# Kernel tuning notes

Hardware: AMD Instinct MI355X
Metric: run time of the kernel (lower is better)

Reference implementation:

```python
import jax, jax.numpy as jnp
import numpy as np

EMBED_DIM = 2048
NUM_HEADS = 16
HEAD_DIM = EMBED_DIM // NUM_HEADS
WINDOW = 512  # window_size; also used as chunk size (S must be a multiple)


def setup_inputs() -> dict:
    key = jax.random.key(0)
    k1, k2, k3 = jax.random.split(key, 3)
    B, S = 2, 4096
    x = jax.random.normal(k1, (B, S, EMBED_DIM), dtype=jnp.float32)
    w_qkv = jax.random.normal(k2, (3 * EMBED_DIM, EMBED_DIM), dtype=jnp.float32) * 0.02
    w_out = jax.random.normal(k3, (EMBED_DIM, EMBED_DIM), dtype=jnp.float32) * 0.02
    return {"x": x, "w_qkv": w_qkv, "w_out": w_out}


def _sliding_window_attn(q, k, v, window):
    # q,k,v: [B,H,S,d]; causal sliding window: kv valid iff 0 <= q_idx - kv_idx <= window.
    # Chunked O(S*window): each query chunk of size C=window attends to its own
    # chunk and the previous one (exactly covers the band of width window+1).
    B, H, S, d = q.shape
    C = window
    nc = S // C
    qc = q.reshape(B, H, nc, C, d)

    def two_chunks(t):
        tc = t.reshape(B, H, nc, C, d)
        prev = jnp.pad(tc[:, :, :-1], ((0, 0), (0, 0), (1, 0), (0, 0), (0, 0)))
        return jnp.concatenate([prev, tc], axis=3)  # [B,H,nc,2C,d]

    kc = two_chunks(k)
    vc = two_chunks(v)

    scale = 1.0 / np.sqrt(d).astype(np.float32)
    scores = jnp.einsum('bhnid,bhnjd->bhnij', qc, kc) * scale  # [B,H,nc,C,2C]

    i = jnp.arange(C)[:, None]            # local query index
    j = jnp.arange(2 * C)[None, :]        # local kv index within the 2-chunk span
    band = (j >= i) & (j <= i + C)        # causal & within window (C == window)
    kv_global = (jnp.arange(nc)[:, None, None] - 1) * C + j[None]  # [nc,1,2C]
    mask = band[None] & (kv_global >= 0)  # [nc,C,2C]; drops padded chunk 0 keys

    scores = jnp.where(mask[None, None], scores, jnp.finfo(scores.dtype).min)
    probs = jax.nn.softmax(scores, axis=-1)
    out = jnp.einsum('bhnij,bhnjd->bhnid', probs, vc)  # [B,H,nc,C,d]
    return out.reshape(B, H, S, d)


def reference(x, w_qkv, w_out):
    B, S, E = x.shape
    qkv = jnp.einsum('bse,fe->bsf', x, w_qkv)                       # [B,S,3E]
    qkv = qkv.reshape(B, S, 3, NUM_HEADS, HEAD_DIM)
    qkv = jnp.transpose(qkv, (2, 0, 3, 1, 4))                        # [3,B,H,S,d]
    q, k, v = qkv[0], qkv[1], qkv[2]
    attn = _sliding_window_attn(q, k, v, WINDOW)                     # [B,H,S,d]
    attn = jnp.transpose(attn, (0, 2, 1, 3)).reshape(B, S, E)
    return jnp.einsum('bse,fe->bsf', attn, w_out)
```

## Files before the change

### kernel.cpp

```cpp
#include <hip/hip_runtime.h>
#include <hip/hip_bf16.h>
#include <math.h>


#define SEQ   4096
#define BATCH 2
#define EMBED 2048
#define HEADS 16
#define HDIM  128
#define NELEM (BATCH * SEQ * EMBED)
#define SCL2E (0.088388347648318447f * 1.4426950408889634f)

typedef __attribute__((ext_vector_type(8))) short short8;
typedef __attribute__((ext_vector_type(4))) float f32x4;

__device__ __forceinline__ unsigned short f2bf(float f) {
    unsigned int u = __float_as_uint(f);
    u = (u + 0x7fff + ((u >> 16) & 1)) >> 16;
    return (unsigned short)u;
}

__device__ __forceinline__ unsigned int cvt_pk_bf16(float a, float b) {
    unsigned int r;
    asm volatile("v_cvt_pk_bf16_f32 %0, %1, %2" : "=v"(r) : "v"(a), "v"(b));
    return r;
}

__global__ void cast_bf16_kernel(const float* __restrict__ src,
                                 unsigned short* __restrict__ dst, int n8)
{
    const int i = blockIdx.x * blockDim.x + threadIdx.x;
    if (i >= n8) return;
    const float4 v0 = ((const float4*)src)[2 * i];
    const float4 v1 = ((const float4*)src)[2 * i + 1];
    union { unsigned short us[8]; uint4 u4; } o;
    o.us[0] = f2bf(v0.x); o.us[1] = f2bf(v0.y); o.us[2] = f2bf(v0.z); o.us[3] = f2bf(v0.w);
    o.us[4] = f2bf(v1.x); o.us[5] = f2bf(v1.y); o.us[6] = f2bf(v1.z); o.us[7] = f2bf(v1.w);
    ((uint4*)dst)[i] = o.u4;
}

template <int MODE>
__global__ __launch_bounds__(512, 2)
void gemm256_kernel(const unsigned short* __restrict__ A,
                    const unsigned short* __restrict__ B,
                    float* __restrict__ C,
                    unsigned short* __restrict__ P0,
                    unsigned short* __restrict__ P1,
                    int M, int N, int K)
{
    __shared__ __align__(16) char lds[131072];

    const int tid  = threadIdx.x;
    const int lane = tid & 63;
    const int w    = tid >> 6;
    const int wm   = w >> 2;
    const int wn   = w & 3;
    const int l16  = lane & 15;
    const int kg   = lane >> 4;

    const int nwg  = gridDim.x * gridDim.y;
    const int bidl = blockIdx.y * gridDim.x + blockIdx.x;
    const int cpx  = nwg >> 3;
    const int swzb = (bidl & 7) * cpx + (bidl >> 3);
    const int m0   = (swzb / gridDim.x) * 256;
    const int n0   = (swzb % gridDim.x) * 256;

    const int srow = w * 8 + (lane >> 3);
    const int sch8 = ((lane & 7) ^ (lane >> 3)) * 8;

    auto stage = [&](const unsigned short* X, int rowbase, int t2, int ldsbase) {
#pragma unroll
        for (int u = 0; u < 2; ++u) {
            const unsigned short* g = X + (size_t)(rowbase + u * 64 + srow) * K
                                      + t2 * 64 + sch8;
            unsigned int lb = __builtin_amdgcn_readfirstlane(
                (unsigned int)(uintptr_t)(lds + ldsbase + u * 8192 + w * 1024));
            asm volatile("s_mov_b32 m0, %0\n\t"
                         "global_load_lds_dwordx4 %1, off"
                         :: "s"(lb), "v"(g) : "memory");
        }
    };
    auto rdA = [&](int p, int mf, int ks) -> short8 {
        return *(const short8*)(lds + p * 65536 + (wm * 128 + mf * 16 + l16) * 128
                                + (((ks * 4 + kg) ^ (l16 & 7)) << 4));
    };
    auto rdB = [&](int p, int nf, int ks) -> short8 {
        return *(const short8*)(lds + 32768 + p * 65536
                                + (wn * 64 + nf * 16 + l16) * 128
                                + (((ks * 4 + kg) ^ (l16 & 7)) << 4));
    };

    f32x4 acc[8][4];
#pragma unroll
    for (int i = 0; i < 8; ++i)
#pragma unroll
        for (int j = 0; j < 4; ++j) acc[i][j] = (f32x4)0.f;

    const int NT = K >> 6;

    stage(B, n0 + 0,   0, 32768);
    stage(B, n0 + 128, 0, 32768 + 16384);
    stage(A, m0 + 0,   0, 0);
    stage(A, m0 + 128, 0, 16384);
    stage(B, n0 + 0,   1, 32768 + 65536);
    stage(B, n0 + 128, 1, 32768 + 65536 + 16384);
    asm volatile("s_waitcnt vmcnt(4)" ::: "memory");
    asm volatile("s_barrier" ::: "memory");

    short8 bfr[4][2];
    for (int t = 0; t < NT; ++t) {
        const int p = t & 1;
#pragma unroll
        for (int q = 0; q < 4; ++q) {
            short8 afr[2][2];
#pragma unroll
            for (int i = 0; i < 2; ++i)
#pragma unroll
                for (int ks = 0; ks < 2; ++ks)
                    afr[i][ks] = rdA(p, 2 * q + i, ks);
            if (q == 0) {
#pragma unroll
                for (int nf = 0; nf < 4; ++nf)
#pragma unroll
                    for (int ks = 0; ks < 2; ++ks)
                        bfr[nf][ks] = rdB(p, nf, ks);
            }
            if (q == 0)      { if (t + 1 < NT) stage(A, m0 + 0,   t + 1, (p ^ 1) * 65536); }
            else if (q == 1) { if (t + 1 < NT) stage(A, m0 + 128, t + 1, (p ^ 1) * 65536 + 16384); }
            else if (q == 2) { if (t + 2 < NT) stage(B, n0 + 0,   t + 2, p * 65536 + 32768); }
            else             { if (t + 2 < NT) stage(B, n0 + 128, t + 2, p * 65536 + 32768 + 16384); }

            asm volatile("s_barrier" ::: "memory");
            __builtin_amdgcn_s_setprio(1);
#pragma unroll
            for (int i = 0; i < 2; ++i)
#pragma unroll
                for (int nf = 0; nf < 4; ++nf)
#pragma unroll
                    for (int ks = 0; ks < 2; ++ks)
                        acc[2 * q + i][nf] = __builtin_amdgcn_mfma_f32_16x16x32_bf16(
                            afr[i][ks], bfr[nf][ks], acc[2 * q + i][nf], 0, 0, 0);
            __builtin_amdgcn_s_setprio(0);
            if (q == 3) {
                if (t >= NT - 2) asm volatile("s_waitcnt vmcnt(0)" ::: "memory");
                else             asm volatile("s_waitcnt vmcnt(4)" ::: "memory");
            }
            asm volatile("s_barrier" ::: "memory");
        }
    }

    if (MODE == 1) {
        const int cb = n0 + wn * 64;
        unsigned short* dst = (cb >> 11) ? P1 : P0;
        const int h  = (cb >> 7) & 15;
        const int db = cb & 127;
#pragma unroll
        for (int fi = 0; fi < 8; ++fi)
#pragma unroll
            for (int r = 0; r < 4; ++r) {
                const int mrow = m0 + wm * 128 + fi * 16 + kg * 4 + r;
                const int b = mrow >> 12, s = mrow & 4095;
                unsigned short* drow = dst + ((size_t)((b << 4) + h) * SEQ + s) * HDIM
                                       + db + l16;
#pragma unroll
                for (int nf = 0; nf < 4; ++nf) drow[nf * 16] = f2bf(acc[fi][nf][r]);
            }
    } else if (MODE == 2) {
#pragma unroll
        for (int fi = 0; fi < 8; ++fi)
#pragma unroll
            for (int r = 0; r < 4; ++r) {
                const int mrow = m0 + wm * 128 + fi * 16 + kg * 4 + r;
                const int h = mrow >> 7, d = mrow & 127;
#pragma unroll
                for (int nf = 0; nf < 4; ++nf) {
                    const int col = n0 + wn * 64 + nf * 16 + l16;
                    const int b = col >> 12, s = col & 4095;
                    const int sl = s & 63;
                    const int c = (sl & 0x23) | ((sl & 0x0C) << 1) | ((sl & 0x10) >> 2);
                    P0[((size_t)((b << 4) + h) * HDIM + d) * SEQ + (s & ~63) + c] =
                        f2bf(acc[fi][nf][r]);
                }
            }
    } else {
#pragma unroll
        for (int fi = 0; fi < 8; ++fi)
#pragma unroll
            for (int r = 0; r < 4; ++r) {
                float* crow = C + (size_t)(m0 + wm * 128 + fi * 16 + kg * 4 + r) * N
                              + n0 + wn * 64 + l16;
#pragma unroll
                for (int nf = 0; nf < 4; ++nf) crow[nf * 16] = acc[fi][nf][r];
            }
    }
}

__global__ __launch_bounds__(512)
void swa_mfma_kernel(const unsigned short* __restrict__ Qg,
                     const unsigned short* __restrict__ Kg,
                     const unsigned short* __restrict__ Vtg,
                     unsigned short* __restrict__ O )
{
    __shared__ __align__(16) char lds[32768];

    const int bid = blockIdx.x;
    const int qt  = bid & 31;
    const int h   = (bid >> 5) & 15;
    const int b   = bid >> 9;
    const int q0  = qt * 128;
    const int tid  = threadIdx.x;
    const int w    = tid >> 6;
    const int lane = tid & 63;
    const int l16  = lane & 15;
    const int kg   = lane >> 4;
    const size_t base = (size_t)((b << 4) + h) * SEQ * HDIM;
    const int gq = q0 + w * 16 + l16;

    short8 qf[4];
#pragma unroll
    for (int kw = 0; kw < 4; ++kw)
        qf[kw] = *(const short8*)(Qg + base + (size_t)gq * HDIM + kw * 32 + kg * 8);

    f32x4 acc_o[8];
#pragma unroll
    for (int db = 0; db < 8; ++db) acc_o[db] = (f32x4)0.f;
    float m = -1e30f, l = 0.f;

    for (int kt = 0; kt < 10; ++kt) {
        const int gk0 = q0 - 512 + kt * 64;
        if (gk0 < 0) continue;

#pragma unroll
        for (int u = 0; u < 2; ++u) {
            {
                const int id  = u * 512 + w * 64 + lane;
                const int row = id >> 4, ch = id & 15;
                const char* g = (const char*)(Kg + base + (size_t)(gk0 + row) * HDIM
                                              + ((ch ^ (row & 7)) << 3));
                unsigned int lb = __builtin_amdgcn_readfirstlane(
                    (unsigned int)(uintptr_t)(lds + u * 8192 + w * 1024));
                asm volatile("s_mov_b32 m0, %0\n\t"
                             "global_load_lds_dwordx4 %1, off"
                             :: "s"(lb), "v"(g) : "memory");
            }
            {
                const int id  = u * 512 + w * 64 + lane;
                const int d   = id >> 3, ch = id & 7;
                const char* g = (const char*)(Vtg + base + (size_t)d * SEQ + gk0
                                              + ((ch ^ (d & 7)) << 3));
                unsigned int lb = __builtin_amdgcn_readfirstlane(
                    (unsigned int)(uintptr_t)(lds + 16384 + u * 8192 + w * 1024));
                asm volatile("s_mov_b32 m0, %0\n\t"
                             "global_load_lds_dwordx4 %1, off"
                             :: "s"(lb), "v"(g) : "memory");
            }
        }
        asm volatile("s_waitcnt vmcnt(0)" ::: "memory");
        __syncthreads();

        const int qlo = q0 + w * 16;
        const bool active = (gk0 <= qlo + 15) && (gk0 + 63 >= qlo - 512);
        if (active) {
            f32x4 s4[4];
#pragma unroll
            for (int kb = 0; kb < 4; ++kb) s4[kb] = (f32x4)0.f;
#pragma unroll
            for (int kw = 0; kw < 4; ++kw)
#pragma unroll
                for (int kb = 0; kb < 4; ++kb) {
                    short8 kf = *(const short8*)(lds + (kb * 16 + l16) * 256
                                                 + (((kw * 4 + kg) ^ (l16 & 7)) << 4));
                    s4[kb] = __builtin_amdgcn_mfma_f32_16x16x32_bf16(
                        kf, qf[kw], s4[kb], 0, 0, 0);
                }

            const int dq = gq - gk0;
            float p[4][4];
            float tm = -1e30f;
#pragma unroll
            for (int kb = 0; kb < 4; ++kb)
#pragma unroll
                for (int r = 0; r < 4; ++r) {
                    const int koff = kb * 16 + kg * 4 + r;
                    const bool valid = (koff <= dq) && (koff >= dq - 512);
                    const float sv = valid ? s4[kb][r] * SCL2E : -1e30f;
                    p[kb][r] = sv;
                    tm = fmaxf(tm, sv);
                }
            tm = fmaxf(tm, __shfl_xor(tm, 16));
            tm = fmaxf(tm, __shfl_xor(tm, 32));
            const float mn   = fmaxf(m, tm);
            const float corr = __builtin_amdgcn_exp2f(m - mn);
            m = mn;
            l *= corr;
            float cr[4];
#pragma unroll
            for (int r = 0; r < 4; ++r) cr[r] = __shfl(corr, kg * 4 + r);
#pragma unroll
            for (int db = 0; db < 8; ++db)
#pragma unroll
                for (int r = 0; r < 4; ++r) acc_o[db][r] *= cr[r];

            float ts = 0.f;
#pragma unroll
            for (int kb = 0; kb < 4; ++kb)
#pragma unroll
                for (int r = 0; r < 4; ++r) {
                    const float pv = (p[kb][r] > -1e29f)
                                         ? __builtin_amdgcn_exp2f(p[kb][r] - m) : 0.f;
                    p[kb][r] = pv;
                    ts += pv;
                }
            ts += __shfl_xor(ts, 16);
            ts += __shfl_xor(ts, 32);
            l += ts;

            unsigned int dw[4][2];
#pragma unroll
            for (int kb = 0; kb < 4; ++kb) {
                dw[kb][0] = cvt_pk_bf16(p[kb][0], p[kb][1]);
                dw[kb][1] = cvt_pk_bf16(p[kb][2], p[kb][3]);
            }
#pragma unroll
            for (int w2 = 0; w2 < 2; ++w2) {
                union { unsigned int u[4]; short8 v; } pu;
                pu.u[0] = dw[2 * w2][0];     pu.u[1] = dw[2 * w2][1];
                pu.u[2] = dw[2 * w2 + 1][0]; pu.u[3] = dw[2 * w2 + 1][1];
#pragma unroll
                for (int db = 0; db < 8; ++db) {
                    short8 vf = *(const short8*)(lds + 16384 + (db * 16 + l16) * 128
                                                 + (((w2 * 4 + kg) ^ (l16 & 7)) << 4));
                    acc_o[db] = __builtin_amdgcn_mfma_f32_16x16x32_bf16(
                        pu.v, vf, acc_o[db], 0, 0, 0);
                }
            }
        }
        __syncthreads();
    }

    const float inv = 1.0f / l;
    float li[4];
#pragma unroll
    for (int r = 0; r < 4; ++r) li[r] = __shfl(inv, kg * 4 + r);
#pragma unroll
    for (int db = 0; db < 8; ++db)
#pragma unroll
        for (int r = 0; r < 4; ++r) {
            const int gqr = q0 + w * 16 + kg * 4 + r;
            O[((size_t)b * SEQ + gqr) * EMBED + h * HDIM + db * 16 + l16] =
                f2bf(acc_o[db][r] * li[r]);
        }
}

extern "C" void kernel_launch(void* const* d_in, const int* in_sizes, int n_in,
                              void* d_out, int out_size, void* d_ws, size_t ws_size,
                              hipStream_t stream)
{
    const float* x     = (const float*)d_in[0];
    const float* w_qkv = (const float*)d_in[1];
    const float* w_out = (const float*)d_in[2];
    float* out = (float*)d_out;

    char* ws = (char*)d_ws;
    unsigned short* xb    = (unsigned short*)(ws);
    unsigned short* wqkvb = (unsigned short*)(ws + 33554432);
    unsigned short* woutb = (unsigned short*)(ws + 58720256);
    unsigned short* qb    = (unsigned short*)(ws + 67108864);
    unsigned short* kb    = (unsigned short*)(ws + 100663296);
    unsigned short* vtb   = (unsigned short*)(ws + 134217728);
    unsigned short* attnb = (unsigned short*)(ws + 167772160);

    const int M = BATCH * SEQ;
    dim3 blk(256);

    hipLaunchKernelGGL(cast_bf16_kernel, dim3(NELEM / 8 / 256), blk, 0, stream,
                       x, xb, NELEM / 8);
    hipLaunchKernelGGL(cast_bf16_kernel, dim3(3 * EMBED * EMBED / 8 / 256), blk, 0, stream,
                       w_qkv, wqkvb, 3 * EMBED * EMBED / 8);
    hipLaunchKernelGGL(cast_bf16_kernel, dim3(EMBED * EMBED / 8 / 256), blk, 0, stream,
                       w_out, woutb, EMBED * EMBED / 8);

    hipLaunchKernelGGL((gemm256_kernel<1>), dim3(16, 32), dim3(512), 0, stream,
                       xb, wqkvb, (float*)nullptr, qb, kb, M, 2 * EMBED, EMBED);

    hipLaunchKernelGGL((gemm256_kernel<2>), dim3(32, 8), dim3(512), 0, stream,
                       wqkvb + (size_t)2 * EMBED * EMBED, xb, (float*)nullptr,
                       vtb, (unsigned short*)nullptr, EMBED, M, EMBED);

    hipLaunchKernelGGL(swa_mfma_kernel, dim3(BATCH * HEADS * (SEQ / 128)), dim3(512),
                       0, stream, qb, kb, vtb, attnb);

    hipLaunchKernelGGL((gemm256_kernel<0>), dim3(8, 32), dim3(512), 0, stream,
                       attnb, woutb, out, (unsigned short*)nullptr,
                       (unsigned short*)nullptr, M, EMBED, EMBED);
}
```

Before: 404.1 us.

## Software-pipeline GEMM fragment loads and double-buffer KV tiles in attention

The GEMM kernel's LDS layout changes to separate A and B double buffers (32KB each), so A fragments for the next quarter and next k-tile load from LDS while the current MFMAs run. It also swaps the block swizzle so consecutive blocks walk down M within an N column. The attention kernel double-buffers its K/V tiles in 64KB of LDS, prefetching the next tile before computing the current one. It also skips fully masked leading tiles by starting at a computed kt and drops the trailing syncthreads. The aim is to hide LDS and global load latency behind MFMA work, at the cost of more registers and LDS, which may lower occupancy.

```diff
diff --git a/kernel.cpp b/kernel.cpp
--- a/kernel.cpp
+++ b/kernel.cpp
@@ -62,8 +62,9 @@
     const int bidl = blockIdx.y * gridDim.x + blockIdx.x;
     const int cpx  = nwg >> 3;
     const int swzb = (bidl & 7) * cpx + (bidl >> 3);
-    const int m0   = (swzb / gridDim.x) * 256;
-    const int n0   = (swzb % gridDim.x) * 256;
+    const int MB   = gridDim.y;
+    const int n0   = (swzb / MB) * 256;
+    const int m0   = (swzb % MB) * 256;
 
     const int srow = w * 8 + (lane >> 3);
     const int sch8 = ((lane & 7) ^ (lane >> 3)) * 8;
@@ -81,11 +82,11 @@
         }
     };
     auto rdA = [&](int p, int mf, int ks) -> short8 {
-        return *(const short8*)(lds + p * 65536 + (wm * 128 + mf * 16 + l16) * 128
+        return *(const short8*)(lds + p * 32768 + (wm * 128 + mf * 16 + l16) * 128
                                 + (((ks * 4 + kg) ^ (l16 & 7)) << 4));
     };
     auto rdB = [&](int p, int nf, int ks) -> short8 {
-        return *(const short8*)(lds + 32768 + p * 65536
+        return *(const short8*)(lds + 65536 + p * 32768
                                 + (wn * 64 + nf * 16 + l16) * 128
                                 + (((ks * 4 + kg) ^ (l16 & 7)) << 4));
     };
@@ -98,56 +99,86 @@
 
     const int NT = K >> 6;
 
-    stage(B, n0 + 0,   0, 32768);
-    stage(B, n0 + 128, 0, 32768 + 16384);
     stage(A, m0 + 0,   0, 0);
     stage(A, m0 + 128, 0, 16384);
-    stage(B, n0 + 0,   1, 32768 + 65536);
-    stage(B, n0 + 128, 1, 32768 + 65536 + 16384);
-    asm volatile("s_waitcnt vmcnt(4)" ::: "memory");
+    stage(B, n0 + 0,   0, 65536);
+    stage(B, n0 + 128, 0, 65536 + 16384);
+    if (NT > 1) {
+        stage(B, n0 + 0,   1, 65536 + 32768);
+        stage(B, n0 + 128, 1, 65536 + 32768 + 16384);
+        asm volatile("s_waitcnt vmcnt(4)" ::: "memory");
+    } else {
+        asm volatile("s_waitcnt vmcnt(0)" ::: "memory");
+    }
     asm volatile("s_barrier" ::: "memory");
 
-    short8 bfr[4][2];
+    short8 afrA[2][2], afrB[2][2], bfr[4][2];
+#pragma unroll
+    for (int i = 0; i < 2; ++i)
+#pragma unroll
+        for (int ks = 0; ks < 2; ++ks) afrA[i][ks] = rdA(0, i, ks);
+#pragma unroll
+    for (int nf = 0; nf < 4; ++nf)
+#pragma unroll
+        for (int ks = 0; ks < 2; ++ks) bfr[nf][ks] = rdB(0, nf, ks);
+
+#define MFMA_QUAD(Q, FR)                                                        \
+    __builtin_amdgcn_s_setprio(1);                                              \
+    _Pragma("unroll")                                                           \
+    for (int i = 0; i < 2; ++i)                                                 \
+        _Pragma("unroll")                                                       \
+        for (int nf = 0; nf < 4; ++nf)                                          \
+            _Pragma("unroll")                                                   \
+            for (int ks = 0; ks < 2; ++ks)                                      \
+                acc[2 * (Q) + i][nf] = __builtin_amdgcn_mfma_f32_16x16x32_bf16( \
+                    FR[i][ks], bfr[nf][ks], acc[2 * (Q) + i][nf], 0, 0, 0);     \
+    __builtin_amdgcn_s_setprio(0);
+
     for (int t = 0; t < NT; ++t) {
         const int p = t & 1;
-#pragma unroll
-        for (int q = 0; q < 4; ++q) {
-            short8 afr[2][2];
+        if (t + 1 < NT) stage(A, m0 + 0, t + 1, (p ^ 1) * 32768);
+        asm volatile("s_barrier" ::: "memory");
+#pragma unroll
+        for (int i = 0; i < 2; ++i)
+#pragma unroll
+            for (int ks = 0; ks < 2; ++ks) afrB[i][ks] = rdA(p, 2 + i, ks);
+        MFMA_QUAD(0, afrA)
+        if (t + 1 < NT) stage(A, m0 + 128, t + 1, (p ^ 1) * 32768 + 16384);
+        asm volatile("s_barrier" ::: "memory");
+#pragma unroll
+        for (int i = 0; i < 2; ++i)
+#pragma unroll
+            for (int ks = 0; ks < 2; ++ks) afrA[i][ks] = rdA(p, 4 + i, ks);
+        MFMA_QUAD(1, afrB)
+        if (t + 2 < NT) stage(B, n0 + 0, t + 2, 65536 + p * 32768);
+        asm volatile("s_barrier" ::: "memory");
+#pragma unroll
+        for (int i = 0; i < 2; ++i)
+#pragma unroll
+            for (int ks = 0; ks < 2; ++ks) afrB[i][ks] = rdA(p, 6 + i, ks);
+        MFMA_QUAD(2, afrA)
+        if (t + 2 < NT) {
+            stage(B, n0 + 128, t + 2, 65536 + p * 32768 + 16384);
+            asm volatile("s_waitcnt vmcnt(4)" ::: "memory");
+        } else {
+            asm volatile("s_waitcnt vmcnt(0)" ::: "memory");
+        }
+        asm volatile("s_barrier" ::: "memory");
+        if (t + 1 < NT) {
 #pragma unroll
             for (int i = 0; i < 2; ++i)
 #pragma unroll
-                for (int ks = 0; ks < 2; ++ks)
-                    afr[i][ks] = rdA(p, 2 * q + i, ks);
-            if (q == 0) {
-#pragma unroll
-                for (int nf = 0; nf < 4; ++nf)
-#pragma unroll
-                    for (int ks = 0; ks < 2; ++ks)
-                        bfr[nf][ks] = rdB(p, nf, ks);
-            }
-            if (q == 0)      { if (t + 1 < NT) stage(A, m0 + 0,   t + 1, (p ^ 1) * 65536); }
-            else if (q == 1) { if (t + 1 < NT) stage(A, m0 + 128, t + 1, (p ^ 1) * 65536 + 16384); }
-            else if (q == 2) { if (t + 2 < NT) stage(B, n0 + 0,   t + 2, p * 65536 + 32768); }
-            else             { if (t + 2 < NT) stage(B, n0 + 128, t + 2, p * 65536 + 32768 + 16384); }
-
-            asm volatile("s_barrier" ::: "memory");
-            __builtin_amdgcn_s_setprio(1);
-#pragma unroll
-            for (int i = 0; i < 2; ++i)
-#pragma unroll
-                for (int nf = 0; nf < 4; ++nf)
-#pragma unroll
-                    for (int ks = 0; ks < 2; ++ks)
-                        acc[2 * q + i][nf] = __builtin_amdgcn_mfma_f32_16x16x32_bf16(
-                            afr[i][ks], bfr[nf][ks], acc[2 * q + i][nf], 0, 0, 0);
-            __builtin_amdgcn_s_setprio(0);
-            if (q == 3) {
-                if (t >= NT - 2) asm volatile("s_waitcnt vmcnt(0)" ::: "memory");
-                else             asm volatile("s_waitcnt vmcnt(4)" ::: "memory");
-            }
-            asm volatile("s_barrier" ::: "memory");
+                for (int ks = 0; ks < 2; ++ks) afrA[i][ks] = rdA(p ^ 1, i, ks);
+        }
+        MFMA_QUAD(3, afrB)
+        if (t + 1 < NT) {
+#pragma unroll
+            for (int nf = 0; nf < 4; ++nf)
+#pragma unroll
+                for (int ks = 0; ks < 2; ++ks) bfr[nf][ks] = rdB(p ^ 1, nf, ks);
         }
     }
+#undef MFMA_QUAD
 
     if (MODE == 1) {
         const int cb = n0 + wn * 64;
@@ -201,7 +232,7 @@
                      const unsigned short* __restrict__ Vtg,
                      unsigned short* __restrict__ O )
 {
-    __shared__ __align__(16) char lds[32768];
+    __shared__ __align__(16) char lds[65536];
 
     const int bid = blockIdx.x;
     const int qt  = bid & 31;
@@ -226,10 +257,8 @@
     for (int db = 0; db < 8; ++db) acc_o[db] = (f32x4)0.f;
     float m = -1e30f, l = 0.f;
 
-    for (int kt = 0; kt < 10; ++kt) {
+    auto stageKV = [&](int kt, int buf) {
         const int gk0 = q0 - 512 + kt * 64;
-        if (gk0 < 0) continue;
-
 #pragma unroll
         for (int u = 0; u < 2; ++u) {
             {
@@ -238,7 +267,7 @@
                 const char* g = (const char*)(Kg + base + (size_t)(gk0 + row) * HDIM
                                               + ((ch ^ (row & 7)) << 3));
                 unsigned int lb = __builtin_amdgcn_readfirstlane(
-                    (unsigned int)(uintptr_t)(lds + u * 8192 + w * 1024));
+                    (unsigned int)(uintptr_t)(lds + buf * 32768 + u * 8192 + w * 1024));
                 asm volatile("s_mov_b32 m0, %0\n\t"
                              "global_load_lds_dwordx4 %1, off"
                              :: "s"(lb), "v"(g) : "memory");
@@ -249,15 +278,26 @@
                 const char* g = (const char*)(Vtg + base + (size_t)d * SEQ + gk0
                                               + ((ch ^ (d & 7)) << 3));
                 unsigned int lb = __builtin_amdgcn_readfirstlane(
-                    (unsigned int)(uintptr_t)(lds + 16384 + u * 8192 + w * 1024));
+                    (unsigned int)(uintptr_t)(lds + buf * 32768 + 16384
+                                              + u * 8192 + w * 1024));
                 asm volatile("s_mov_b32 m0, %0\n\t"
                              "global_load_lds_dwordx4 %1, off"
                              :: "s"(lb), "v"(g) : "memory");
             }
         }
+    };
+
+    const int kt_start = (qt < 4) ? (8 - 2 * qt) : 0;
+    stageKV(kt_start, 0);
+    int cur = 0;
+
+    for (int kt = kt_start; kt < 10; ++kt) {
         asm volatile("s_waitcnt vmcnt(0)" ::: "memory");
         __syncthreads();
-
+        if (kt + 1 < 10) stageKV(kt + 1, cur ^ 1);
+
+        const int gk0 = q0 - 512 + kt * 64;
+        const char* ldsb = lds + cur * 32768;
         const int qlo = q0 + w * 16;
         const bool active = (gk0 <= qlo + 15) && (gk0 + 63 >= qlo - 512);
         if (active) {
@@ -268,7 +308,7 @@
             for (int kw = 0; kw < 4; ++kw)
 #pragma unroll
                 for (int kb = 0; kb < 4; ++kb) {
-                    short8 kf = *(const short8*)(lds + (kb * 16 + l16) * 256
+                    short8 kf = *(const short8*)(ldsb + (kb * 16 + l16) * 256
                                                  + (((kw * 4 + kg) ^ (l16 & 7)) << 4));
                     s4[kb] = __builtin_amdgcn_mfma_f32_16x16x32_bf16(
                         kf, qf[kw], s4[kb], 0, 0, 0);
@@ -328,14 +368,14 @@
                 pu.u[2] = dw[2 * w2 + 1][0]; pu.u[3] = dw[2 * w2 + 1][1];
 #pragma unroll
                 for (int db = 0; db < 8; ++db) {
-                    short8 vf = *(const short8*)(lds + 16384 + (db * 16 + l16) * 128
+                    short8 vf = *(const short8*)(ldsb + 16384 + (db * 16 + l16) * 128
                                                  + (((w2 * 4 + kg) ^ (l16 & 7)) << 4));
                     acc_o[db] = __builtin_amdgcn_mfma_f32_16x16x32_bf16(
                         pu.v, vf, acc_o[db], 0, 0, 0);
                 }
             }
         }
-        __syncthreads();
+        cur ^= 1;
     }
 
     const float inv = 1.0f / l;
```

Result: faster. 356.1 us (-11.9%).

## Load GEMM B fragments directly to registers and double-buffer SWA K/V tiles

Applied to the files above, without the earlier changes.

The GEMM now stages only the A tile through LDS (halving LDS to 64KB) and loads B operands straight from global memory into double-buffered register fragments. The main loop is restructured into one prefetch-then-compute step per K tile with a single barrier, replacing the four-phase interleaved staging. The sliding-window attention kernel gets a double-buffered K/V LDS pipeline that prefetches the next tile while computing the current one, and it starts at the first valid tile instead of skipping via continue. The aim is to cut barrier count and hide load latency, at the cost of uncoalesced, L2-heavy B loads and higher register pressure now that the occupancy hint is dropped.

```diff
diff --git a/kernel.cpp b/kernel.cpp
--- a/kernel.cpp
+++ b/kernel.cpp
@@ -40,7 +40,7 @@
 }
 
 template <int MODE>
-__global__ __launch_bounds__(512, 2)
+__global__ __launch_bounds__(512)
 void gemm256_kernel(const unsigned short* __restrict__ A,
                     const unsigned short* __restrict__ B,
                     float* __restrict__ C,
@@ -48,7 +48,7 @@
                     unsigned short* __restrict__ P1,
                     int M, int N, int K)
 {
-    __shared__ __align__(16) char lds[131072];
+    __shared__ __align__(16) char lds[65536];
 
     const int tid  = threadIdx.x;
     const int lane = tid & 63;
@@ -68,26 +68,31 @@
     const int srow = w * 8 + (lane >> 3);
     const int sch8 = ((lane & 7) ^ (lane >> 3)) * 8;
 
-    auto stage = [&](const unsigned short* X, int rowbase, int t2, int ldsbase) {
+    auto stageA = [&](int half, int t2, int p) {
 #pragma unroll
         for (int u = 0; u < 2; ++u) {
-            const unsigned short* g = X + (size_t)(rowbase + u * 64 + srow) * K
+            const unsigned short* g = A + (size_t)(m0 + half * 128 + u * 64 + srow) * K
                                       + t2 * 64 + sch8;
             unsigned int lb = __builtin_amdgcn_readfirstlane(
-                (unsigned int)(uintptr_t)(lds + ldsbase + u * 8192 + w * 1024));
+                (unsigned int)(uintptr_t)(lds + p * 32768 + half * 16384
+                                          + u * 8192 + w * 1024));
             asm volatile("s_mov_b32 m0, %0\n\t"
                          "global_load_lds_dwordx4 %1, off"
                          :: "s"(lb), "v"(g) : "memory");
         }
     };
     auto rdA = [&](int p, int mf, int ks) -> short8 {
-        return *(const short8*)(lds + p * 65536 + (wm * 128 + mf * 16 + l16) * 128
+        return *(const short8*)(lds + p * 32768 + (wm * 128 + mf * 16 + l16) * 128
                                 + (((ks * 4 + kg) ^ (l16 & 7)) << 4));
     };
-    auto rdB = [&](int p, int nf, int ks) -> short8 {
-        return *(const short8*)(lds + 32768 + p * 65536
-                                + (wn * 64 + nf * 16 + l16) * 128
-                                + (((ks * 4 + kg) ^ (l16 & 7)) << 4));
+    auto loadB = [&](short8 (&dst)[4][2], int t2) {
+#pragma unroll
+        for (int nf = 0; nf < 4; ++nf)
+#pragma unroll
+            for (int ks = 0; ks < 2; ++ks)
+                dst[nf][ks] = *(const short8*)(B
+                    + (size_t)(n0 + wn * 64 + nf * 16 + l16) * K
+                    + t2 * 64 + ks * 32 + kg * 8);
     };
 
     f32x4 acc[8][4];
@@ -98,55 +103,42 @@
 
     const int NT = K >> 6;
 
-    stage(B, n0 + 0,   0, 32768);
-    stage(B, n0 + 128, 0, 32768 + 16384);
-    stage(A, m0 + 0,   0, 0);
-    stage(A, m0 + 128, 0, 16384);
-    stage(B, n0 + 0,   1, 32768 + 65536);
-    stage(B, n0 + 128, 1, 32768 + 65536 + 16384);
-    asm volatile("s_waitcnt vmcnt(4)" ::: "memory");
-    asm volatile("s_barrier" ::: "memory");
-
-    short8 bfr[4][2];
-    for (int t = 0; t < NT; ++t) {
+    short8 bA[4][2], bB[4][2];
+
+    loadB(bA, 0);
+    stageA(0, 0, 0);
+    stageA(1, 0, 0);
+    asm volatile("s_waitcnt vmcnt(0)" ::: "memory");
+    __syncthreads();
+
+    auto tile = [&](int t, short8 (&cur)[4][2], short8 (&nxt)[4][2]) {
         const int p = t & 1;
-#pragma unroll
-        for (int q = 0; q < 4; ++q) {
-            short8 afr[2][2];
-#pragma unroll
-            for (int i = 0; i < 2; ++i)
-#pragma unroll
-                for (int ks = 0; ks < 2; ++ks)
-                    afr[i][ks] = rdA(p, 2 * q + i, ks);
-            if (q == 0) {
-#pragma unroll
-                for (int nf = 0; nf < 4; ++nf)
-#pragma unroll
-                    for (int ks = 0; ks < 2; ++ks)
-                        bfr[nf][ks] = rdB(p, nf, ks);
-            }
-            if (q == 0)      { if (t + 1 < NT) stage(A, m0 + 0,   t + 1, (p ^ 1) * 65536); }
-            else if (q == 1) { if (t + 1 < NT) stage(A, m0 + 128, t + 1, (p ^ 1) * 65536 + 16384); }
-            else if (q == 2) { if (t + 2 < NT) stage(B, n0 + 0,   t + 2, p * 65536 + 32768); }
-            else             { if (t + 2 < NT) stage(B, n0 + 128, t + 2, p * 65536 + 32768 + 16384); }
-
-            asm volatile("s_barrier" ::: "memory");
-            __builtin_amdgcn_s_setprio(1);
-#pragma unroll
-            for (int i = 0; i < 2; ++i)
-#pragma unroll
-                for (int nf = 0; nf < 4; ++nf)
-#pragma unroll
-                    for (int ks = 0; ks < 2; ++ks)
-                        acc[2 * q + i][nf] = __builtin_amdgcn_mfma_f32_16x16x32_bf16(
-                            afr[i][ks], bfr[nf][ks], acc[2 * q + i][nf], 0, 0, 0);
-            __builtin_amdgcn_s_setprio(0);
-            if (q == 3) {
-                if (t >= NT - 2) asm volatile("s_waitcnt vmcnt(0)" ::: "memory");
-                else             asm volatile("s_waitcnt vmcnt(4)" ::: "memory");
-            }
-            asm volatile("s_barrier" ::: "memory");
-        }
+        if (t + 1 < NT) {
+            stageA(0, t + 1, p ^ 1);
+            stageA(1, t + 1, p ^ 1);
+            loadB(nxt, t + 1);
+        }
+        __builtin_amdgcn_s_setprio(1);
+#pragma unroll
+        for (int mf = 0; mf < 8; ++mf) {
+            const short8 a0 = rdA(p, mf, 0);
+            const short8 a1 = rdA(p, mf, 1);
+#pragma unroll
+            for (int nf = 0; nf < 4; ++nf) {
+                acc[mf][nf] = __builtin_amdgcn_mfma_f32_16x16x32_bf16(
+                    a0, cur[nf][0], acc[mf][nf], 0, 0, 0);
+                acc[mf][nf] = __builtin_amdgcn_mfma_f32_16x16x32_bf16(
+                    a1, cur[nf][1], acc[mf][nf], 0, 0, 0);
+            }
+        }
+        __builtin_amdgcn_s_setprio(0);
+        asm volatile("s_waitcnt vmcnt(0)" ::: "memory");
+        __syncthreads();
+    };
+
+    for (int t = 0; t < NT; t += 2) {
+        tile(t, bA, bB);
+        tile(t + 1, bB, bA);
     }
 
     if (MODE == 1) {
@@ -201,7 +193,7 @@
                      const unsigned short* __restrict__ Vtg,
                      unsigned short* __restrict__ O )
 {
-    __shared__ __align__(16) char lds[32768];
+    __shared__ __align__(16) char lds[65536];
 
     const int bid = blockIdx.x;
     const int qt  = bid & 31;
@@ -226,10 +218,8 @@
     for (int db = 0; db < 8; ++db) acc_o[db] = (f32x4)0.f;
     float m = -1e30f, l = 0.f;
 
-    for (int kt = 0; kt < 10; ++kt) {
+    auto stageKV = [&](int kt, int buf) {
         const int gk0 = q0 - 512 + kt * 64;
-        if (gk0 < 0) continue;
-
 #pragma unroll
         for (int u = 0; u < 2; ++u) {
             {
@@ -238,7 +228,7 @@
                 const char* g = (const char*)(Kg + base + (size_t)(gk0 + row) * HDIM
                                               + ((ch ^ (row & 7)) << 3));
                 unsigned int lb = __builtin_amdgcn_readfirstlane(
-                    (unsigned int)(uintptr_t)(lds + u * 8192 + w * 1024));
+                    (unsigned int)(uintptr_t)(lds + buf * 32768 + u * 8192 + w * 1024));
                 asm volatile("s_mov_b32 m0, %0\n\t"
                              "global_load_lds_dwordx4 %1, off"
                              :: "s"(lb), "v"(g) : "memory");
@@ -249,15 +239,26 @@
                 const char* g = (const char*)(Vtg + base + (size_t)d * SEQ + gk0
                                               + ((ch ^ (d & 7)) << 3));
                 unsigned int lb = __builtin_amdgcn_readfirstlane(
-                    (unsigned int)(uintptr_t)(lds + 16384 + u * 8192 + w * 1024));
+                    (unsigned int)(uintptr_t)(lds + buf * 32768 + 16384
+                                              + u * 8192 + w * 1024));
                 asm volatile("s_mov_b32 m0, %0\n\t"
                              "global_load_lds_dwordx4 %1, off"
                              :: "s"(lb), "v"(g) : "memory");
             }
         }
+    };
+
+    const int kt_start = (qt < 4) ? (8 - 2 * qt) : 0;
+    stageKV(kt_start, 0);
+    int cur = 0;
+
+    for (int kt = kt_start; kt < 10; ++kt) {
         asm volatile("s_waitcnt vmcnt(0)" ::: "memory");
         __syncthreads();
-
+        if (kt + 1 < 10) stageKV(kt + 1, cur ^ 1);
+
+        const int gk0 = q0 - 512 + kt * 64;
+        const char* ldsb = lds + cur * 32768;
         const int qlo = q0 + w * 16;
         const bool active = (gk0 <= qlo + 15) && (gk0 + 63 >= qlo - 512);
         if (active) {
@@ -268,7 +269,7 @@
             for (int kw = 0; kw < 4; ++kw)
 #pragma unroll
                 for (int kb = 0; kb < 4; ++kb) {
-                    short8 kf = *(const short8*)(lds + (kb * 16 + l16) * 256
+                    short8 kf = *(const short8*)(ldsb + (kb * 16 + l16) * 256
                                                  + (((kw * 4 + kg) ^ (l16 & 7)) << 4));
                     s4[kb] = __builtin_amdgcn_mfma_f32_16x16x32_bf16(
                         kf, qf[kw], s4[kb], 0, 0, 0);
@@ -328,14 +329,14 @@
                 pu.u[2] = dw[2 * w2 + 1][0]; pu.u[3] = dw[2 * w2 + 1][1];
 #pragma unroll
                 for (int db = 0; db < 8; ++db) {
-                    short8 vf = *(const short8*)(lds + 16384 + (db * 16 + l16) * 128
+                    short8 vf = *(const short8*)(ldsb + 16384 + (db * 16 + l16) * 128
                                                  + (((w2 * 4 + kg) ^ (l16 & 7)) << 4));
                     acc_o[db] = __builtin_amdgcn_mfma_f32_16x16x32_bf16(
                         pu.v, vf, acc_o[db], 0, 0, 0);
                 }
             }
         }
-        __syncthreads();
+        cur ^= 1;
     }
 
     const float inv = 1.0f / l;
```

After: 482.5 us. +19.4%, slower.
